# Kernel optimization log

Measured on AMD Instinct MI355X. Metric: run time of the kernel, lower is better.

The kernel has to match this reference:

```python
import jax, jax.numpy as jnp
import numpy as np

N_NODES = 50000
N_EDGES = 800000
IN_DIM = 128
HID = 96
OUT_DIM = 128
N_LAYERS = 3


def setup_inputs() -> dict:
    key = jax.random.key(0)
    ks = jax.random.split(key, 10)
    x = jax.random.normal(ks[0], (N_NODES, IN_DIM), dtype=jnp.float32)
    edge_index = jax.random.randint(ks[1], (2, N_EDGES), 0, N_NODES, dtype=jnp.int32)
    s = 1.0 / np.sqrt(IN_DIM)
    W_in = jax.random.uniform(ks[2], (HID, IN_DIM), jnp.float32, -s, s)
    b_in = jax.random.uniform(ks[3], (HID,), jnp.float32, -s, s)
    sh = 1.0 / np.sqrt(HID)
    W_layers = jax.random.uniform(ks[4], (N_LAYERS, HID, HID), jnp.float32, -sh, sh)
    b_layers = jax.random.uniform(ks[5], (N_LAYERS, HID), jnp.float32, -sh, sh)
    sc = 1.0 / np.sqrt((N_LAYERS + 1) * HID)
    W_out = jax.random.uniform(ks[6], (OUT_DIM, (N_LAYERS + 1) * HID), jnp.float32, -sc, sc)
    b_out = jax.random.uniform(ks[7], (OUT_DIM,), jnp.float32, -sc, sc)
    return {"x": x, "edge_index": edge_index, "W_in": W_in, "b_in": b_in,
            "W_layers": W_layers, "b_layers": b_layers, "W_out": W_out, "b_out": b_out}


def reference(x, edge_index, W_in, b_in, W_layers, b_layers, W_out, b_out):
    src, dst = edge_index[0], edge_index[1]
    # input projection
    h = x @ W_in.T + b_in  # [N, HID]
    hidden_states = [h]
    for l in range(N_LAYERS):
        # GINConv (eps=0): nn((1+eps)*x_i + sum_{j in N(i)} x_j)
        agg = jax.ops.segment_sum(h[src], dst, num_segments=N_NODES)  # [N, HID]
        h = (h + agg) @ W_layers[l].T + b_layers[l]
        hidden_states.append(h)
    cat = jnp.concatenate(hidden_states, axis=1)  # [N, (L+1)*HID]
    return cat @ W_out.T + b_out
```

## Files before the change

kernel.cpp:

```cpp
#include <hip/hip_runtime.h>

#define NN   50000
#define NE   800000
#define IND  128
#define HIDD 96
#define OUTD 128
#define CATD (4 * HIDD)
#define CAP  64

typedef __attribute__((ext_vector_type(8))) short short8v;
typedef __attribute__((ext_vector_type(4))) float f32x4;

__device__ __forceinline__ ushort f2bf(float f) {
    unsigned u = __float_as_uint(f);
    u = (u + 0x7FFFu + ((u >> 16) & 1u)) >> 16;
    return (ushort)u;
}
__device__ __forceinline__ float bf2f(ushort h) {
    return __uint_as_float(((unsigned)h) << 16);
}
__device__ __forceinline__ float blo(unsigned u) { return __uint_as_float(u << 16); }
__device__ __forceinline__ float bhi(unsigned u) { return __uint_as_float(u & 0xffff0000u); }

#define NW_IN  (HIDD * IND)
#define NW_L   (3 * HIDD * HIDD)
#define NW_OUT (OUTD * CATD)
#define NW_ROW (NW_IN + NW_L + NW_OUT)
#define NW_ALL (NW_ROW + NW_L + NW_OUT)

__global__ __launch_bounds__(256)
void wsplit_k(const float* __restrict__ Wi, const float* __restrict__ Wl,
              const float* __restrict__ Wo,
              ushort* __restrict__ whi, ushort* __restrict__ wlo)
{
    int i = blockIdx.x * 256 + threadIdx.x;
    if (i >= NW_ALL) return;
    float v;
    if (i < NW_ROW) {
        if (i < NW_IN)              v = Wi[i];
        else if (i < NW_IN + NW_L)  v = Wl[i - NW_IN];
        else                        v = Wo[i - NW_IN - NW_L];
    } else if (i < NW_ROW + NW_L) {
        int fi = i - NW_ROW;
        int l  = fi / 9216;
        int r  = fi - l * 9216;
        int c  = r / 1536;
        int ks = (r % 1536) / 512;
        int ln = (r % 512) / 8;
        int t  = r & 7;
        int j  = c * 16 + (ln & 15);
        int k  = ks * 32 + 8 * (ln >> 4) + t;
        v = Wl[(l * HIDD + j) * HIDD + k];
    } else {
        int fi = i - NW_ROW - NW_L;
        int c  = fi / 6144;
        int r  = fi - c * 6144;
        int ks = r / 512;
        int ln = (r % 512) / 8;
        int t  = r & 7;
        int j  = c * 16 + (ln & 15);
        int k  = ks * 32 + 8 * (ln >> 4) + t;
        v = Wo[j * CATD + k];
    }
    ushort h = f2bf(v);
    whi[i] = h;
    wlo[i] = f2bf(v - bf2f(h));
}

template<int K, int NCOLS, int ROWS, bool ACCUM>
__global__ __launch_bounds__(256)
void mgemm_k(const float* __restrict__ A,
             const ushort* __restrict__ Whi, const ushort* __restrict__ Wlo,
             int wstride, const float* __restrict__ bias,
             float* __restrict__ C, int cstride, int nrows)
{
    constexpr int ST  = K + 8;
    constexpr int KS  = K / 32;
    constexpr int TRP = (ROWS / 16) / 2;
    constexpr int TCP = (NCOLS / 16) / 2;
    constexpr int CPR = K / 8;

    __shared__ __align__(16) ushort sWh[NCOLS * ST];
    __shared__ __align__(16) ushort sWl[NCOLS * ST];

    const int tid  = threadIdx.x;
    const int w    = tid >> 6;
    const int l    = tid & 63;
    const int lr   = l & 15;
    const int lg   = l >> 4;
    const int row0 = blockIdx.x * ROWS;

    for (int idx = tid; idx < NCOLS * CPR; idx += 256) {
        int j = idx / CPR, c = idx - j * CPR;
        *(uint4*)&sWh[j * ST + c * 8] = *(const uint4*)&Whi[(long)j * wstride + c * 8];
        *(uint4*)&sWl[j * ST + c * 8] = *(const uint4*)&Wlo[(long)j * wstride + c * 8];
    }

    short8v Ah[TRP][KS], Al[TRP][KS];
#pragma unroll
    for (int i = 0; i < TRP; i++) {
        const int row = row0 + ((w >> 1) + 2 * i) * 16 + lr;
#pragma unroll
        for (int ks = 0; ks < KS; ks++) {
            float4 r0 = make_float4(0.f, 0.f, 0.f, 0.f);
            float4 r1 = make_float4(0.f, 0.f, 0.f, 0.f);
            if (row < nrows) {
                const float* p = &A[(long)row * K + ks * 32 + 8 * lg];
                r0 = *(const float4*)p;
                r1 = *(const float4*)(p + 4);
            }
            const float f[8] = {r0.x, r0.y, r0.z, r0.w, r1.x, r1.y, r1.z, r1.w};
            short8v hi, lo;
#pragma unroll
            for (int t = 0; t < 8; t++) {
                ushort h = f2bf(f[t]);
                hi[t] = (short)h;
                lo[t] = (short)f2bf(f[t] - bf2f(h));
            }
            Ah[i][ks] = hi;
            Al[i][ks] = lo;
        }
    }
    __syncthreads();

#pragma unroll
    for (int j = 0; j < TCP; j++) {
        const int colb = ((w & 1) + 2 * j) * 16;
        short8v Bh[KS], Bl[KS];
#pragma unroll
        for (int ks = 0; ks < KS; ks++) {
            Bh[ks] = *(const short8v*)&sWh[(colb + lr) * ST + ks * 32 + 8 * lg];
            Bl[ks] = *(const short8v*)&sWl[(colb + lr) * ST + ks * 32 + 8 * lg];
        }
        const float bv = bias ? bias[colb + lr] : 0.f;
#pragma unroll
        for (int i = 0; i < TRP; i++) {
            f32x4 acc = {bv, bv, bv, bv};
#pragma unroll
            for (int ks = 0; ks < KS; ks++) {
                acc = __builtin_amdgcn_mfma_f32_16x16x32_bf16(Ah[i][ks], Bh[ks], acc, 0, 0, 0);
                acc = __builtin_amdgcn_mfma_f32_16x16x32_bf16(Ah[i][ks], Bl[ks], acc, 0, 0, 0);
                acc = __builtin_amdgcn_mfma_f32_16x16x32_bf16(Al[i][ks], Bh[ks], acc, 0, 0, 0);
            }
#pragma unroll
            for (int p = 0; p < 4; p++) {
                const int row = row0 + ((w >> 1) + 2 * i) * 16 + 4 * lg + p;
                if (row < nrows) {
                    float* cp = &C[(long)row * cstride + colb + lr];
                    if (ACCUM) *cp += acc[p];
                    else       *cp  = acc[p];
                }
            }
        }
    }
}

__global__ __launch_bounds__(256)
void fillb_k(const int* __restrict__ ei, int* __restrict__ cursor,
             ushort* __restrict__ bucket)
{
    unsigned int e = blockIdx.x * 256u + threadIdx.x;
    if (e < (unsigned int)NE) {
        int s = ei[e];
        int d = ei[NE + e];
        int pos = atomicAdd(&cursor[d], 1);
        if (pos < CAP) bucket[(long)d * CAP + pos] = (ushort)s;
    }
}

__global__ __launch_bounds__(256)
void hcvt_k(const float* __restrict__ hf, int istride, ushort* __restrict__ hb)
{
    int idx = blockIdx.x * 256 + threadIdx.x;
    if (idx >= NN * (HIDD / 8)) return;
    int row = idx / (HIDD / 8);
    int c   = (idx - row * (HIDD / 8)) * 8;
    const float* p = &hf[(long)row * istride + c];
    const float4 r0 = *(const float4*)p;
    const float4 r1 = *(const float4*)(p + 4);
    uint4 o;
    o.x = (unsigned)f2bf(r0.x) | ((unsigned)f2bf(r0.y) << 16);
    o.y = (unsigned)f2bf(r0.z) | ((unsigned)f2bf(r0.w) << 16);
    o.z = (unsigned)f2bf(r1.x) | ((unsigned)f2bf(r1.y) << 16);
    o.w = (unsigned)f2bf(r1.z) | ((unsigned)f2bf(r1.w) << 16);
    *(uint4*)&hb[(long)row * HIDD + c] = o;
}

#define FROWS 32
#define FAST  100

__global__ __launch_bounds__(256)
void flayer_k(const float* __restrict__ hf_in, int istride,
              const ushort* __restrict__ hb_in,
              const int* __restrict__ cursor, const ushort* __restrict__ bucket,
              const ushort* __restrict__ fWhi, const ushort* __restrict__ fWlo,
              const float* __restrict__ bias,
              float* __restrict__ hf_out, int ostride,
              ushort* __restrict__ hb_out)
{
    __shared__ __align__(16) float sA[FROWS * FAST];

    const int tid = threadIdx.x;
    const int n0  = blockIdx.x * FROWS;

    {
        const int i  = tid >> 3;
        const int st = tid & 7;
        const int n  = n0 + i;
        float4 s0 = make_float4(0.f, 0.f, 0.f, 0.f);
        float4 s1 = s0, s2 = s0;
        if (n < NN) {
            const float* hp = &hf_in[(long)n * istride + st * 12];
            s0 = ((const float4*)hp)[0];
            s1 = *(const float4*)(hp + 4);
            s2 = *(const float4*)(hp + 8);
            int cnt = cursor[n];
            if (cnt > CAP) cnt = CAP;
            const ushort* bp = &bucket[(long)n * CAP];
            const ushort* hbb = hb_in + st * 12;
#define ACCB(q)                                                              \
            { const uint2 a = *(const uint2*)(q);                            \
              const uint2 b = *(const uint2*)((q) + 4);                      \
              const uint2 c = *(const uint2*)((q) + 8);                      \
              s0.x += blo(a.x); s0.y += bhi(a.x); s0.z += blo(a.y); s0.w += bhi(a.y); \
              s1.x += blo(b.x); s1.y += bhi(b.x); s1.z += blo(b.y); s1.w += bhi(b.y); \
              s2.x += blo(c.x); s2.y += bhi(c.x); s2.z += blo(c.y); s2.w += bhi(c.y); }
            int e = 0;
            for (; e + 1 < cnt; e += 2) {
                const unsigned id2 = *(const unsigned*)&bp[e];
                const ushort* q0 = &hbb[(long)(id2 & 0xffffu) * HIDD];
                const ushort* q1 = &hbb[(long)(id2 >> 16) * HIDD];
                ACCB(q0); ACCB(q1);
            }
            if (e < cnt) {
                const ushort* q = &hbb[(long)bp[e] * HIDD];
                ACCB(q);
            }
#undef ACCB
        }
        float* ap = &sA[i * FAST + st * 12];
        ((float4*)ap)[0] = s0;
        ((float4*)ap)[1] = s1;
        ((float4*)ap)[2] = s2;
    }
    __syncthreads();

    const int w  = tid >> 6;
    const int l  = tid & 63;
    const int lr = l & 15;
    const int lg = l >> 4;
    const int tr = w >> 1;

    short8v Ah[3], Al[3];
#pragma unroll
    for (int ks = 0; ks < 3; ks++) {
        const float* ap = &sA[(tr * 16 + lr) * FAST + ks * 32 + 8 * lg];
        const float4 r0 = ((const float4*)ap)[0];
        const float4 r1 = ((const float4*)ap)[1];
        const float f[8] = {r0.x, r0.y, r0.z, r0.w, r1.x, r1.y, r1.z, r1.w};
        short8v hi, lo;
#pragma unroll
        for (int t = 0; t < 8; t++) {
            ushort h = f2bf(f[t]);
            hi[t] = (short)h;
            lo[t] = (short)f2bf(f[t] - bf2f(h));
        }
        Ah[ks] = hi;
        Al[ks] = lo;
    }

#pragma unroll
    for (int j = 0; j < 3; j++) {
        const int c    = (w & 1) + 2 * j;
        const int colb = c * 16;
        short8v Bh[3], Bl[3];
#pragma unroll
        for (int ks = 0; ks < 3; ks++) {
            Bh[ks] = *(const short8v*)&fWhi[((c * 3 + ks) * 64 + l) * 8];
            Bl[ks] = *(const short8v*)&fWlo[((c * 3 + ks) * 64 + l) * 8];
        }
        const float bv = bias[colb + lr];
        f32x4 acc = {bv, bv, bv, bv};
#pragma unroll
        for (int ks = 0; ks < 3; ks++) {
            acc = __builtin_amdgcn_mfma_f32_16x16x32_bf16(Ah[ks], Bh[ks], acc, 0, 0, 0);
            acc = __builtin_amdgcn_mfma_f32_16x16x32_bf16(Ah[ks], Bl[ks], acc, 0, 0, 0);
            acc = __builtin_amdgcn_mfma_f32_16x16x32_bf16(Al[ks], Bh[ks], acc, 0, 0, 0);
        }
#pragma unroll
        for (int p = 0; p < 4; p++) {
            const int row = n0 + tr * 16 + 4 * lg + p;
            if (row < NN) {
                hf_out[(long)row * ostride + colb + lr] = acc[p];
                if (hb_out)
                    hb_out[(long)row * HIDD + colb + lr] = f2bf(acc[p]);
            }
        }
    }
}

__global__ __launch_bounds__(256)
void fgemm_k(const float* __restrict__ cat, const ushort* __restrict__ fOhi,
             const ushort* __restrict__ fOlo, const float* __restrict__ bias,
             float* __restrict__ out)
{
    const int tid  = threadIdx.x;
    const int w    = tid >> 6;
    const int l    = tid & 63;
    const int lr   = l & 15;
    const int lg   = l >> 4;
    const int row0 = blockIdx.x * 32;
    const int rt   = w >> 1;
    const int ch   = w & 1;
    const int arow = row0 + rt * 16 + lr;

    f32x4 acc[4];
#pragma unroll
    for (int j = 0; j < 4; j++) {
        const float bv = bias[(ch + 2 * j) * 16 + lr];
        acc[j] = (f32x4){bv, bv, bv, bv};
    }

#pragma unroll 4
    for (int ks = 0; ks < 12; ks++) {
        float4 r0 = make_float4(0.f, 0.f, 0.f, 0.f);
        float4 r1 = make_float4(0.f, 0.f, 0.f, 0.f);
        if (arow < NN) {
            const float* p = &cat[(long)arow * CATD + ks * 32 + 8 * lg];
            r0 = *(const float4*)p;
            r1 = *(const float4*)(p + 4);
        }
        const float f[8] = {r0.x, r0.y, r0.z, r0.w, r1.x, r1.y, r1.z, r1.w};
        short8v Ah, Al;
#pragma unroll
        for (int t = 0; t < 8; t++) {
            ushort h = f2bf(f[t]);
            Ah[t] = (short)h;
            Al[t] = (short)f2bf(f[t] - bf2f(h));
        }
#pragma unroll
        for (int j = 0; j < 4; j++) {
            const int c = ch + 2 * j;
            const short8v Bh = *(const short8v*)&fOhi[((c * 12 + ks) * 64 + l) * 8];
            const short8v Bl = *(const short8v*)&fOlo[((c * 12 + ks) * 64 + l) * 8];
            acc[j] = __builtin_amdgcn_mfma_f32_16x16x32_bf16(Ah, Bh, acc[j], 0, 0, 0);
            acc[j] = __builtin_amdgcn_mfma_f32_16x16x32_bf16(Ah, Bl, acc[j], 0, 0, 0);
            acc[j] = __builtin_amdgcn_mfma_f32_16x16x32_bf16(Al, Bh, acc[j], 0, 0, 0);
        }
    }

#pragma unroll
    for (int p = 0; p < 4; p++) {
        const int row = row0 + rt * 16 + 4 * lg + p;
        if (row < NN) {
#pragma unroll
            for (int j = 0; j < 4; j++)
                out[(long)row * OUTD + (ch + 2 * j) * 16 + lr] = acc[j][p];
        }
    }
}

extern "C" void kernel_launch(void* const* d_in, const int* in_sizes, int n_in,
                              void* d_out, int out_size, void* d_ws, size_t ws_size,
                              hipStream_t stream)
{
    const float* x  = (const float*)d_in[0];
    const int*   ei = (const int*)  d_in[1];
    const float* Wi = (const float*)d_in[2];
    const float* bi = (const float*)d_in[3];
    const float* Wl = (const float*)d_in[4];
    const float* bl = (const float*)d_in[5];
    const float* Wo = (const float*)d_in[6];
    const float* bo = (const float*)d_in[7];
    float* out = (float*)d_out;

    char* p = (char*)d_ws;
    int* cursor    = (int*)p;              p += ((size_t)NN * 4 + 255) & ~255ull;
    ushort* bucket = (ushort*)p;           p += ((size_t)NN * CAP * 2 + 255) & ~255ull;
    ushort* whi = (ushort*)p;              p += ((size_t)NW_ALL * 2 + 255) & ~255ull;
    ushort* wlo = (ushort*)p;              p += ((size_t)NW_ALL * 2 + 255) & ~255ull;
    ushort* hbfA = (ushort*)p;             p += ((size_t)NN * HIDD * 2 + 255) & ~255ull;
    ushort* hbfB = (ushort*)p;             p += ((size_t)NN * HIDD * 2 + 255) & ~255ull;
    float* big  = (float*)p;
    const size_t used = (size_t)(p - (char*)d_ws);
    const bool catpath = (ws_size >= used + (size_t)NN * CATD * 4);

    const ushort* whi_in = whi;
    const ushort* wlo_in = wlo;
    const ushort* whi_o  = whi + NW_IN + NW_L;
    const ushort* wlo_o  = wlo + NW_IN + NW_L;
    const ushort* fLhi   = whi + NW_ROW;
    const ushort* fLlo   = wlo + NW_ROW;
    const ushort* fOhi   = whi + NW_ROW + NW_L;
    const ushort* fOlo   = wlo + NW_ROW + NW_L;

    hipLaunchKernelGGL(wsplit_k, dim3((NW_ALL + 255) / 256), dim3(256), 0, stream,
                       Wi, Wl, Wo, whi, wlo);
    hipMemsetAsync(cursor, 0, (size_t)NN * sizeof(int), stream);
    hipLaunchKernelGGL(fillb_k, dim3((NE + 255) / 256), dim3(256), 0, stream,
                       ei, cursor, bucket);

    if (catpath) {
        float* cat = big;
        hipLaunchKernelGGL((mgemm_k<IND, HIDD, 32, false>),
                           dim3((NN + 31) / 32), dim3(256), 0, stream,
                           x, whi_in, wlo_in, IND, bi, cat, CATD, NN);
        hipLaunchKernelGGL(hcvt_k, dim3((NN * (HIDD / 8) + 255) / 256), dim3(256), 0, stream,
                           cat, CATD, hbfA);
        hipLaunchKernelGGL(flayer_k, dim3((NN + FROWS - 1) / FROWS), dim3(256), 0, stream,
                           cat, CATD, hbfA, cursor, bucket,
                           fLhi, fLlo, bl, cat + HIDD, CATD, hbfB);
        hipLaunchKernelGGL(flayer_k, dim3((NN + FROWS - 1) / FROWS), dim3(256), 0, stream,
                           cat + HIDD, CATD, hbfB, cursor, bucket,
                           fLhi + 9216, fLlo + 9216, bl + HIDD,
                           cat + 2 * HIDD, CATD, hbfA);
        hipLaunchKernelGGL(flayer_k, dim3((NN + FROWS - 1) / FROWS), dim3(256), 0, stream,
                           cat + 2 * HIDD, CATD, hbfA, cursor, bucket,
                           fLhi + 2 * 9216, fLlo + 2 * 9216, bl + 2 * HIDD,
                           cat + 3 * HIDD, CATD, (ushort*)nullptr);
        hipLaunchKernelGGL(fgemm_k, dim3((NN + 31) / 32), dim3(256), 0, stream,
                           cat, fOhi, fOlo, bo, out);
    } else {
        float* hA = big;
        float* hB = hA + (size_t)NN * HIDD;
        hipLaunchKernelGGL((mgemm_k<IND, HIDD, 32, false>),
                           dim3((NN + 31) / 32), dim3(256), 0, stream,
                           x, whi_in, wlo_in, IND, bi, hA, HIDD, NN);
        hipLaunchKernelGGL((mgemm_k<HIDD, OUTD, 64, false>),
                           dim3((NN + 63) / 64), dim3(256), 0, stream,
                           hA, whi_o, wlo_o, CATD, bo, out, OUTD, NN);
        hipLaunchKernelGGL(hcvt_k, dim3((NN * (HIDD / 8) + 255) / 256), dim3(256), 0, stream,
                           hA, HIDD, hbfA);
        const float* hsrc = hA;  float* hdst = hB;
        ushort* bsrc = hbfA;     ushort* bdst = hbfB;
        for (int l = 0; l < 3; l++) {
            hipLaunchKernelGGL(flayer_k, dim3((NN + FROWS - 1) / FROWS), dim3(256), 0, stream,
                               hsrc, HIDD, bsrc, cursor, bucket,
                               fLhi + (size_t)l * 9216, fLlo + (size_t)l * 9216,
                               bl + (size_t)l * HIDD, hdst, HIDD,
                               (l < 2) ? bdst : (ushort*)nullptr);
            hipLaunchKernelGGL((mgemm_k<HIDD, OUTD, 64, true>),
                               dim3((NN + 63) / 64), dim3(256), 0, stream,
                               hdst, whi_o + (size_t)(l + 1) * HIDD,
                               wlo_o + (size_t)(l + 1) * HIDD, CATD,
                               (const float*)nullptr, out, OUTD, NN);
            const float* t = hsrc; hsrc = hdst; hdst = (float*)t;
            ushort* tb = bsrc; bsrc = bdst; bdst = tb;
        }
    }
}
```

Before: 316.9 us.

## Bin edges by destination before bucket fill and fuse bf16 conversion into GEMM

Replaces the direct per-edge atomic bucket fill with a multi-pass scheme: a shared-memory histogram over 49 destination bins, a scan, a block-local binning pass that writes packed (dst,src) edges grouped by bin, then a per-bin fill so cursor atomics and bucket writes stay localized. It also removes the separate hcvt kernel by having the input-projection GEMM write the bf16 copy directly. The cost is four extra launches, an extra 3.2 MB intermediate array, and a bucket fill limited to 49 blocks. Packing src into 16 bits only works because node ids are below 65536.

Result: slower. 334.9 us (+5.7%).

```diff
diff --git a/kernel.cpp b/kernel.cpp
--- a/kernel.cpp
+++ b/kernel.cpp
@@ -7,6 +7,8 @@
 #define OUTD 128
 #define CATD (4 * HIDD)
 #define CAP  64
+#define NBIN 49
+#define BCH  4096
 
 typedef __attribute__((ext_vector_type(8))) short short8v;
 typedef __attribute__((ext_vector_type(4))) float f32x4;
@@ -72,7 +74,8 @@
 void mgemm_k(const float* __restrict__ A,
              const ushort* __restrict__ Whi, const ushort* __restrict__ Wlo,
              int wstride, const float* __restrict__ bias,
-             float* __restrict__ C, int cstride, int nrows)
+             float* __restrict__ C, int cstride, int nrows,
+             ushort* __restrict__ bfC)
 {
     constexpr int ST  = K + 8;
     constexpr int KS  = K / 32;
@@ -149,6 +152,8 @@
                     float* cp = &C[(long)row * cstride + colb + lr];
                     if (ACCUM) *cp += acc[p];
                     else       *cp  = acc[p];
+                    if (bfC)
+                        bfC[(long)row * HIDD + colb + lr] = f2bf(acc[p]);
                 }
             }
         }
@@ -156,34 +161,106 @@
 }
 
 __global__ __launch_bounds__(256)
-void fillb_k(const int* __restrict__ ei, int* __restrict__ cursor,
-             ushort* __restrict__ bucket)
-{
-    unsigned int e = blockIdx.x * 256u + threadIdx.x;
-    if (e < (unsigned int)NE) {
-        int s = ei[e];
-        int d = ei[NE + e];
-        int pos = atomicAdd(&cursor[d], 1);
+void hist_k(const int* __restrict__ ei, int* __restrict__ binCount)
+{
+    __shared__ int h[NBIN];
+    for (int b = threadIdx.x; b < NBIN; b += 256) h[b] = 0;
+    __syncthreads();
+    int e0 = (blockIdx.x * 256 + threadIdx.x) * 4;
+    if (e0 + 4 <= NE) {
+        const int4 d4 = *(const int4*)&ei[NE + e0];
+        atomicAdd(&h[d4.x >> 10], 1);
+        atomicAdd(&h[d4.y >> 10], 1);
+        atomicAdd(&h[d4.z >> 10], 1);
+        atomicAdd(&h[d4.w >> 10], 1);
+    }
+    __syncthreads();
+    for (int b = threadIdx.x; b < NBIN; b += 256)
+        if (h[b]) atomicAdd(&binCount[b], h[b]);
+}
+
+__global__ __launch_bounds__(64)
+void binscan_k(const int* __restrict__ binCount, int* __restrict__ binStart,
+               int* __restrict__ binCursor)
+{
+    __shared__ int v[64];
+    const int t = threadIdx.x;
+    int x = (t < NBIN) ? binCount[t] : 0;
+    v[t] = x;
+    __syncthreads();
+    for (int off = 1; off < 64; off <<= 1) {
+        int tmp = (t >= off) ? v[t - off] : 0;
+        __syncthreads();
+        v[t] += tmp;
+        __syncthreads();
+    }
+    if (t < NBIN) { int ex = v[t] - x; binStart[t] = ex; binCursor[t] = ex; }
+    if (t == NBIN - 1) binStart[NBIN] = v[t];
+}
+
+__global__ __launch_bounds__(256)
+void binfill_k(const int* __restrict__ ei, int* __restrict__ binCursor,
+               unsigned* __restrict__ binned)
+{
+    __shared__ unsigned sbuf[BCH];
+    __shared__ int lcnt[NBIN], lstart[NBIN], lcur[NBIN], gbase[NBIN];
+    const int tid  = threadIdx.x;
+    const int base = blockIdx.x * BCH;
+
+    for (int b = tid; b < NBIN; b += 256) { lcnt[b] = 0; lcur[b] = 0; }
+    __syncthreads();
+
+    unsigned ent[16];
+#pragma unroll
+    for (int r = 0; r < 16; r++) {
+        const int e = base + r * 256 + tid;
+        if (e < NE) {
+            const int s = ei[e];
+            const int d = ei[NE + e];
+            ent[r] = ((unsigned)d << 16) | (unsigned)s;
+            atomicAdd(&lcnt[d >> 10], 1);
+        } else {
+            ent[r] = 0xffffffffu;
+        }
+    }
+    __syncthreads();
+    if (tid == 0) {
+        int run = 0;
+        for (int b = 0; b < NBIN; b++) { lstart[b] = run; run += lcnt[b]; }
+    }
+    __syncthreads();
+    if (tid < NBIN) gbase[tid] = atomicAdd(&binCursor[tid], lcnt[tid]);
+    __syncthreads();
+#pragma unroll
+    for (int r = 0; r < 16; r++) {
+        if (ent[r] != 0xffffffffu) {
+            const int bin = ent[r] >> 26;
+            const int pos = atomicAdd(&lcur[bin], 1);
+            sbuf[lstart[bin] + pos] = ent[r];
+        }
+    }
+    __syncthreads();
+    const int total = lstart[NBIN - 1] + lcnt[NBIN - 1];
+    for (int i = tid; i < total; i += 256) {
+        const unsigned e = sbuf[i];
+        const int bin = e >> 26;
+        binned[gbase[bin] + (i - lstart[bin])] = e;
+    }
+}
+
+__global__ __launch_bounds__(1024)
+void bfill_k(const unsigned* __restrict__ binned, const int* __restrict__ binStart,
+             int* __restrict__ cursor, ushort* __restrict__ bucket)
+{
+    const int b   = blockIdx.x;
+    const int beg = binStart[b], end = binStart[b + 1];
+    for (int i = beg + threadIdx.x; i < end; i += 1024) {
+        const unsigned e = binned[i];
+        const int d = e >> 16;
+        const int s = e & 0xffffu;
+        const int pos = atomicAdd(&cursor[d], 1);
         if (pos < CAP) bucket[(long)d * CAP + pos] = (ushort)s;
     }
-}
-
-__global__ __launch_bounds__(256)
-void hcvt_k(const float* __restrict__ hf, int istride, ushort* __restrict__ hb)
-{
-    int idx = blockIdx.x * 256 + threadIdx.x;
-    if (idx >= NN * (HIDD / 8)) return;
-    int row = idx / (HIDD / 8);
-    int c   = (idx - row * (HIDD / 8)) * 8;
-    const float* p = &hf[(long)row * istride + c];
-    const float4 r0 = *(const float4*)p;
-    const float4 r1 = *(const float4*)(p + 4);
-    uint4 o;
-    o.x = (unsigned)f2bf(r0.x) | ((unsigned)f2bf(r0.y) << 16);
-    o.y = (unsigned)f2bf(r0.z) | ((unsigned)f2bf(r0.w) << 16);
-    o.z = (unsigned)f2bf(r1.x) | ((unsigned)f2bf(r1.y) << 16);
-    o.w = (unsigned)f2bf(r1.z) | ((unsigned)f2bf(r1.w) << 16);
-    *(uint4*)&hb[(long)row * HIDD + c] = o;
 }
 
 #define FROWS 32
@@ -375,8 +452,12 @@
     float* out = (float*)d_out;
 
     char* p = (char*)d_ws;
-    int* cursor    = (int*)p;              p += ((size_t)NN * 4 + 255) & ~255ull;
+    int* cursor    = (int*)p;              p += ((size_t)(NN + 2 * NBIN + NBIN + 1) * 4 + 255) & ~255ull;
+    int* binCount  = cursor + NN;
+    int* binCursor = binCount + NBIN;
+    int* binStart  = binCursor + NBIN;
     ushort* bucket = (ushort*)p;           p += ((size_t)NN * CAP * 2 + 255) & ~255ull;
+    unsigned* binned = (unsigned*)p;       p += ((size_t)NE * 4 + 255) & ~255ull;
     ushort* whi = (ushort*)p;              p += ((size_t)NW_ALL * 2 + 255) & ~255ull;
     ushort* wlo = (ushort*)p;              p += ((size_t)NW_ALL * 2 + 255) & ~255ull;
     ushort* hbfA = (ushort*)p;             p += ((size_t)NN * HIDD * 2 + 255) & ~255ull;
@@ -396,17 +477,21 @@
 
     hipLaunchKernelGGL(wsplit_k, dim3((NW_ALL + 255) / 256), dim3(256), 0, stream,
                        Wi, Wl, Wo, whi, wlo);
-    hipMemsetAsync(cursor, 0, (size_t)NN * sizeof(int), stream);
-    hipLaunchKernelGGL(fillb_k, dim3((NE + 255) / 256), dim3(256), 0, stream,
-                       ei, cursor, bucket);
+    hipMemsetAsync(cursor, 0, (size_t)(NN + 2 * NBIN) * sizeof(int), stream);
+    hipLaunchKernelGGL(hist_k, dim3((NE / 4 + 255) / 256), dim3(256), 0, stream,
+                       ei, binCount);
+    hipLaunchKernelGGL(binscan_k, dim3(1), dim3(64), 0, stream,
+                       binCount, binStart, binCursor);
+    hipLaunchKernelGGL(binfill_k, dim3((NE + BCH - 1) / BCH), dim3(256), 0, stream,
+                       ei, binCursor, binned);
+    hipLaunchKernelGGL(bfill_k, dim3(NBIN), dim3(1024), 0, stream,
+                       binned, binStart, cursor, bucket);
 
     if (catpath) {
         float* cat = big;
         hipLaunchKernelGGL((mgemm_k<IND, HIDD, 32, false>),
                            dim3((NN + 31) / 32), dim3(256), 0, stream,
-                           x, whi_in, wlo_in, IND, bi, cat, CATD, NN);
-        hipLaunchKernelGGL(hcvt_k, dim3((NN * (HIDD / 8) + 255) / 256), dim3(256), 0, stream,
-                           cat, CATD, hbfA);
+                           x, whi_in, wlo_in, IND, bi, cat, CATD, NN, hbfA);
         hipLaunchKernelGGL(flayer_k, dim3((NN + FROWS - 1) / FROWS), dim3(256), 0, stream,
                            cat, CATD, hbfA, cursor, bucket,
                            fLhi, fLlo, bl, cat + HIDD, CATD, hbfB);
@@ -425,12 +510,10 @@
         float* hB = hA + (size_t)NN * HIDD;
         hipLaunchKernelGGL((mgemm_k<IND, HIDD, 32, false>),
                            dim3((NN + 31) / 32), dim3(256), 0, stream,
-                           x, whi_in, wlo_in, IND, bi, hA, HIDD, NN);
+                           x, whi_in, wlo_in, IND, bi, hA, HIDD, NN, hbfA);
         hipLaunchKernelGGL((mgemm_k<HIDD, OUTD, 64, false>),
                            dim3((NN + 63) / 64), dim3(256), 0, stream,
-                           hA, whi_o, wlo_o, CATD, bo, out, OUTD, NN);
-        hipLaunchKernelGGL(hcvt_k, dim3((NN * (HIDD / 8) + 255) / 256), dim3(256), 0, stream,
-                           hA, HIDD, hbfA);
+                           hA, whi_o, wlo_o, CATD, bo, out, OUTD, NN, (ushort*)nullptr);
         const float* hsrc = hA;  float* hdst = hB;
         ushort* bsrc = hbfA;     ushort* bdst = hbfB;
         for (int l = 0; l < 3; l++) {
@@ -443,7 +526,7 @@
                                dim3((NN + 63) / 64), dim3(256), 0, stream,
                                hdst, whi_o + (size_t)(l + 1) * HIDD,
                                wlo_o + (size_t)(l + 1) * HIDD, CATD,
-                               (const float*)nullptr, out, OUTD, NN);
+                               (const float*)nullptr, out, OUTD, NN, (ushort*)nullptr);
             const float* t = hsrc; hsrc = hdst; hdst = (float*)t;
             ushort* tb = bsrc; bsrc = bdst; bdst = tb;
         }
```

## Store concatenated hidden states as bf16 hi/lo pairs and drop conversion kernel

Applied to the files above, without the earlier changes.

Replaces the fp32 concatenated hidden-state buffer with two bf16 buffers (hi and lo split) written directly by the GEMM and layer kernels. This removes the separate hcvt conversion pass and the per-element fp32-to-bf16 splitting in the output GEMM. The output GEMM is retiled to 64 rows per block with 4x2 MFMA accumulators per wave to reuse B fragments. Neighbor gathers now read from the strided hi buffer inside the cat layout, which may reduce locality compared to the old packed 96-wide bf16 copy.

Result: slower. 341.9 us (+7.9%).

```diff
diff --git a/kernel.cpp b/kernel.cpp
--- a/kernel.cpp
+++ b/kernel.cpp
@@ -72,7 +72,8 @@
 void mgemm_k(const float* __restrict__ A,
              const ushort* __restrict__ Whi, const ushort* __restrict__ Wlo,
              int wstride, const float* __restrict__ bias,
-             float* __restrict__ C, int cstride, int nrows)
+             float* __restrict__ C, int cstride, int nrows,
+             ushort* __restrict__ bfHi, ushort* __restrict__ bfLo, int bstride)
 {
     constexpr int ST  = K + 8;
     constexpr int KS  = K / 32;
@@ -146,9 +147,17 @@
             for (int p = 0; p < 4; p++) {
                 const int row = row0 + ((w >> 1) + 2 * i) * 16 + 4 * lg + p;
                 if (row < nrows) {
-                    float* cp = &C[(long)row * cstride + colb + lr];
-                    if (ACCUM) *cp += acc[p];
-                    else       *cp  = acc[p];
+                    if (C) {
+                        float* cp = &C[(long)row * cstride + colb + lr];
+                        if (ACCUM) *cp += acc[p];
+                        else       *cp  = acc[p];
+                    }
+                    if (bfHi) {
+                        ushort h = f2bf(acc[p]);
+                        bfHi[(long)row * bstride + colb + lr] = h;
+                        if (bfLo)
+                            bfLo[(long)row * bstride + colb + lr] = f2bf(acc[p] - bf2f(h));
+                    }
                 }
             }
         }
@@ -168,35 +177,19 @@
     }
 }
 
-__global__ __launch_bounds__(256)
-void hcvt_k(const float* __restrict__ hf, int istride, ushort* __restrict__ hb)
-{
-    int idx = blockIdx.x * 256 + threadIdx.x;
-    if (idx >= NN * (HIDD / 8)) return;
-    int row = idx / (HIDD / 8);
-    int c   = (idx - row * (HIDD / 8)) * 8;
-    const float* p = &hf[(long)row * istride + c];
-    const float4 r0 = *(const float4*)p;
-    const float4 r1 = *(const float4*)(p + 4);
-    uint4 o;
-    o.x = (unsigned)f2bf(r0.x) | ((unsigned)f2bf(r0.y) << 16);
-    o.y = (unsigned)f2bf(r0.z) | ((unsigned)f2bf(r0.w) << 16);
-    o.z = (unsigned)f2bf(r1.x) | ((unsigned)f2bf(r1.y) << 16);
-    o.w = (unsigned)f2bf(r1.z) | ((unsigned)f2bf(r1.w) << 16);
-    *(uint4*)&hb[(long)row * HIDD + c] = o;
-}
-
 #define FROWS 32
 #define FAST  100
 
 __global__ __launch_bounds__(256)
-void flayer_k(const float* __restrict__ hf_in, int istride,
-              const ushort* __restrict__ hb_in,
+void flayer_k(const float* __restrict__ hf_in, int ifstride,
+              const ushort* __restrict__ hiIn, const ushort* __restrict__ loIn,
+              int ibstride,
               const int* __restrict__ cursor, const ushort* __restrict__ bucket,
               const ushort* __restrict__ fWhi, const ushort* __restrict__ fWlo,
               const float* __restrict__ bias,
-              float* __restrict__ hf_out, int ostride,
-              ushort* __restrict__ hb_out)
+              float* __restrict__ hf_out, int ofstride,
+              ushort* __restrict__ hiOut, ushort* __restrict__ loOut,
+              int obstride)
 {
     __shared__ __align__(16) float sA[FROWS * FAST];
 
@@ -210,14 +203,31 @@
         float4 s0 = make_float4(0.f, 0.f, 0.f, 0.f);
         float4 s1 = s0, s2 = s0;
         if (n < NN) {
-            const float* hp = &hf_in[(long)n * istride + st * 12];
-            s0 = ((const float4*)hp)[0];
-            s1 = *(const float4*)(hp + 4);
-            s2 = *(const float4*)(hp + 8);
+            if (hf_in) {
+                const float* hp = &hf_in[(long)n * ifstride + st * 12];
+                s0 = ((const float4*)hp)[0];
+                s1 = *(const float4*)(hp + 4);
+                s2 = *(const float4*)(hp + 8);
+            } else {
+                const ushort* hq = &hiIn[(long)n * ibstride + st * 12];
+                const ushort* lq = &loIn[(long)n * ibstride + st * 12];
+                const uint2 a = *(const uint2*)hq;
+                const uint2 b = *(const uint2*)(hq + 4);
+                const uint2 c = *(const uint2*)(hq + 8);
+                const uint2 d = *(const uint2*)lq;
+                const uint2 e = *(const uint2*)(lq + 4);
+                const uint2 f = *(const uint2*)(lq + 8);
+                s0 = make_float4(blo(a.x) + blo(d.x), bhi(a.x) + bhi(d.x),
+                                 blo(a.y) + blo(d.y), bhi(a.y) + bhi(d.y));
+                s1 = make_float4(blo(b.x) + blo(e.x), bhi(b.x) + bhi(e.x),
+                                 blo(b.y) + blo(e.y), bhi(b.y) + bhi(e.y));
+                s2 = make_float4(blo(c.x) + blo(f.x), bhi(c.x) + bhi(f.x),
+                                 blo(c.y) + blo(f.y), bhi(c.y) + bhi(f.y));
+            }
             int cnt = cursor[n];
             if (cnt > CAP) cnt = CAP;
             const ushort* bp = &bucket[(long)n * CAP];
-            const ushort* hbb = hb_in + st * 12;
+            const ushort* hbb = hiIn + st * 12;
 #define ACCB(q)                                                              \
             { const uint2 a = *(const uint2*)(q);                            \
               const uint2 b = *(const uint2*)((q) + 4);                      \
@@ -228,12 +238,12 @@
             int e = 0;
             for (; e + 1 < cnt; e += 2) {
                 const unsigned id2 = *(const unsigned*)&bp[e];
-                const ushort* q0 = &hbb[(long)(id2 & 0xffffu) * HIDD];
-                const ushort* q1 = &hbb[(long)(id2 >> 16) * HIDD];
+                const ushort* q0 = &hbb[(long)(id2 & 0xffffu) * ibstride];
+                const ushort* q1 = &hbb[(long)(id2 >> 16) * ibstride];
                 ACCB(q0); ACCB(q1);
             }
             if (e < cnt) {
-                const ushort* q = &hbb[(long)bp[e] * HIDD];
+                const ushort* q = &hbb[(long)bp[e] * ibstride];
                 ACCB(q);
             }
 #undef ACCB
@@ -291,71 +301,78 @@
         for (int p = 0; p < 4; p++) {
             const int row = n0 + tr * 16 + 4 * lg + p;
             if (row < NN) {
-                hf_out[(long)row * ostride + colb + lr] = acc[p];
-                if (hb_out)
-                    hb_out[(long)row * HIDD + colb + lr] = f2bf(acc[p]);
+                if (hf_out)
+                    hf_out[(long)row * ofstride + colb + lr] = acc[p];
+                if (hiOut) {
+                    ushort h = f2bf(acc[p]);
+                    hiOut[(long)row * obstride + colb + lr] = h;
+                    if (loOut)
+                        loOut[(long)row * obstride + colb + lr] = f2bf(acc[p] - bf2f(h));
+                }
             }
         }
     }
 }
 
 __global__ __launch_bounds__(256)
-void fgemm_k(const float* __restrict__ cat, const ushort* __restrict__ fOhi,
-             const ushort* __restrict__ fOlo, const float* __restrict__ bias,
-             float* __restrict__ out)
+void fgemm_k(const ushort* __restrict__ catHi, const ushort* __restrict__ catLo,
+             const ushort* __restrict__ fOhi, const ushort* __restrict__ fOlo,
+             const float* __restrict__ bias, float* __restrict__ out)
 {
     const int tid  = threadIdx.x;
     const int w    = tid >> 6;
     const int l    = tid & 63;
     const int lr   = l & 15;
     const int lg   = l >> 4;
-    const int row0 = blockIdx.x * 32;
-    const int rt   = w >> 1;
-    const int ch   = w & 1;
-    const int arow = row0 + rt * 16 + lr;
-
-    f32x4 acc[4];
-#pragma unroll
-    for (int j = 0; j < 4; j++) {
-        const float bv = bias[(ch + 2 * j) * 16 + lr];
-        acc[j] = (f32x4){bv, bv, bv, bv};
-    }
-
-#pragma unroll 4
+    const int row0 = blockIdx.x * 64;
+
+    f32x4 acc[4][2];
+#pragma unroll
+    for (int cj = 0; cj < 2; cj++) {
+        const float bv = bias[(2 * w + cj) * 16 + lr];
+#pragma unroll
+        for (int rt = 0; rt < 4; rt++) acc[rt][cj] = (f32x4){bv, bv, bv, bv};
+    }
+
+#pragma unroll 3
     for (int ks = 0; ks < 12; ks++) {
-        float4 r0 = make_float4(0.f, 0.f, 0.f, 0.f);
-        float4 r1 = make_float4(0.f, 0.f, 0.f, 0.f);
-        if (arow < NN) {
-            const float* p = &cat[(long)arow * CATD + ks * 32 + 8 * lg];
-            r0 = *(const float4*)p;
-            r1 = *(const float4*)(p + 4);
-        }
-        const float f[8] = {r0.x, r0.y, r0.z, r0.w, r1.x, r1.y, r1.z, r1.w};
-        short8v Ah, Al;
-#pragma unroll
-        for (int t = 0; t < 8; t++) {
-            ushort h = f2bf(f[t]);
-            Ah[t] = (short)h;
-            Al[t] = (short)f2bf(f[t] - bf2f(h));
-        }
-#pragma unroll
-        for (int j = 0; j < 4; j++) {
-            const int c = ch + 2 * j;
+        short8v Ah[4], Al[4];
+#pragma unroll
+        for (int rt = 0; rt < 4; rt++) {
+            const int row = row0 + rt * 16 + lr;
+            if (row < NN) {
+                const long off = (long)row * CATD + ks * 32 + 8 * lg;
+                Ah[rt] = *(const short8v*)&catHi[off];
+                Al[rt] = *(const short8v*)&catLo[off];
+            } else {
+                Ah[rt] = (short8v){0,0,0,0,0,0,0,0};
+                Al[rt] = (short8v){0,0,0,0,0,0,0,0};
+            }
+        }
+#pragma unroll
+        for (int cj = 0; cj < 2; cj++) {
+            const int c = 2 * w + cj;
             const short8v Bh = *(const short8v*)&fOhi[((c * 12 + ks) * 64 + l) * 8];
             const short8v Bl = *(const short8v*)&fOlo[((c * 12 + ks) * 64 + l) * 8];
-            acc[j] = __builtin_amdgcn_mfma_f32_16x16x32_bf16(Ah, Bh, acc[j], 0, 0, 0);
-            acc[j] = __builtin_amdgcn_mfma_f32_16x16x32_bf16(Ah, Bl, acc[j], 0, 0, 0);
-            acc[j] = __builtin_amdgcn_mfma_f32_16x16x32_bf16(Al, Bh, acc[j], 0, 0, 0);
-        }
-    }
-
-#pragma unroll
-    for (int p = 0; p < 4; p++) {
-        const int row = row0 + rt * 16 + 4 * lg + p;
-        if (row < NN) {
-#pragma unroll
-            for (int j = 0; j < 4; j++)
-                out[(long)row * OUTD + (ch + 2 * j) * 16 + lr] = acc[j][p];
+#pragma unroll
+            for (int rt = 0; rt < 4; rt++) {
+                acc[rt][cj] = __builtin_amdgcn_mfma_f32_16x16x32_bf16(Ah[rt], Bh, acc[rt][cj], 0, 0, 0);
+                acc[rt][cj] = __builtin_amdgcn_mfma_f32_16x16x32_bf16(Ah[rt], Bl, acc[rt][cj], 0, 0, 0);
+                acc[rt][cj] = __builtin_amdgcn_mfma_f32_16x16x32_bf16(Al[rt], Bh, acc[rt][cj], 0, 0, 0);
+            }
+        }
+    }
+
+#pragma unroll
+    for (int rt = 0; rt < 4; rt++) {
+#pragma unroll
+        for (int p = 0; p < 4; p++) {
+            const int row = row0 + rt * 16 + 4 * lg + p;
+            if (row < NN) {
+#pragma unroll
+                for (int cj = 0; cj < 2; cj++)
+                    out[(long)row * OUTD + (2 * w + cj) * 16 + lr] = acc[rt][cj][p];
+            }
         }
     }
 }
@@ -379,11 +396,9 @@
     ushort* bucket = (ushort*)p;           p += ((size_t)NN * CAP * 2 + 255) & ~255ull;
     ushort* whi = (ushort*)p;              p += ((size_t)NW_ALL * 2 + 255) & ~255ull;
     ushort* wlo = (ushort*)p;              p += ((size_t)NW_ALL * 2 + 255) & ~255ull;
-    ushort* hbfA = (ushort*)p;             p += ((size_t)NN * HIDD * 2 + 255) & ~255ull;
-    ushort* hbfB = (ushort*)p;             p += ((size_t)NN * HIDD * 2 + 255) & ~255ull;
-    float* big  = (float*)p;
+    char* big = p;
     const size_t used = (size_t)(p - (char*)d_ws);
-    const bool catpath = (ws_size >= used + (size_t)NN * CATD * 4);
+    const bool catpath = (ws_size >= used + 2 * (size_t)NN * CATD * 2);
 
     const ushort* whi_in = whi;
     const ushort* wlo_in = wlo;
@@ -401,49 +416,54 @@
                        ei, cursor, bucket);
 
     if (catpath) {
-        float* cat = big;
+        ushort* catHi = (ushort*)big;
+        ushort* catLo = catHi + (size_t)NN * CATD;
         hipLaunchKernelGGL((mgemm_k<IND, HIDD, 32, false>),
                            dim3((NN + 31) / 32), dim3(256), 0, stream,
-                           x, whi_in, wlo_in, IND, bi, cat, CATD, NN);
-        hipLaunchKernelGGL(hcvt_k, dim3((NN * (HIDD / 8) + 255) / 256), dim3(256), 0, stream,
-                           cat, CATD, hbfA);
-        hipLaunchKernelGGL(flayer_k, dim3((NN + FROWS - 1) / FROWS), dim3(256), 0, stream,
-                           cat, CATD, hbfA, cursor, bucket,
-                           fLhi, fLlo, bl, cat + HIDD, CATD, hbfB);
-        hipLaunchKernelGGL(flayer_k, dim3((NN + FROWS - 1) / FROWS), dim3(256), 0, stream,
-                           cat + HIDD, CATD, hbfB, cursor, bucket,
-                           fLhi + 9216, fLlo + 9216, bl + HIDD,
-                           cat + 2 * HIDD, CATD, hbfA);
-        hipLaunchKernelGGL(flayer_k, dim3((NN + FROWS - 1) / FROWS), dim3(256), 0, stream,
-                           cat + 2 * HIDD, CATD, hbfA, cursor, bucket,
-                           fLhi + 2 * 9216, fLlo + 2 * 9216, bl + 2 * HIDD,
-                           cat + 3 * HIDD, CATD, (ushort*)nullptr);
-        hipLaunchKernelGGL(fgemm_k, dim3((NN + 31) / 32), dim3(256), 0, stream,
-                           cat, fOhi, fOlo, bo, out);
+                           x, whi_in, wlo_in, IND, bi,
+                           (float*)nullptr, 0, NN, catHi, catLo, CATD);
+        for (int l = 0; l < 3; l++) {
+            hipLaunchKernelGGL(flayer_k, dim3((NN + FROWS - 1) / FROWS), dim3(256), 0, stream,
+                               (const float*)nullptr, 0,
+                               catHi + (size_t)l * HIDD, catLo + (size_t)l * HIDD, CATD,
+                               cursor, bucket,
+                               fLhi + (size_t)l * 9216, fLlo + (size_t)l * 9216,
+                               bl + (size_t)l * HIDD,
+                               (float*)nullptr, 0,
+                               catHi + (size_t)(l + 1) * HIDD,
+                               catLo + (size_t)(l + 1) * HIDD, CATD);
+        }
+        hipLaunchKernelGGL(fgemm_k, dim3((NN + 63) / 64), dim3(256), 0, stream,
+                           catHi, catLo, fOhi, fOlo, bo, out);
     } else {
-        float* hA = big;
+        float* hA = (float*)big;
         float* hB = hA + (size_t)NN * HIDD;
+        ushort* hbfA = (ushort*)(hB + (size_t)NN * HIDD);
+        ushort* hbfB = hbfA + (size_t)NN * HIDD;
         hipLaunchKernelGGL((mgemm_k<IND, HIDD, 32, false>),
                            dim3((NN + 31) / 32), dim3(256), 0, stream,
-                           x, whi_in, wlo_in, IND, bi, hA, HIDD, NN);
+                           x, whi_in, wlo_in, IND, bi, hA, HIDD, NN,
+                           hbfA, (ushort*)nullptr, HIDD);
         hipLaunchKernelGGL((mgemm_k<HIDD, OUTD, 64, false>),
                            dim3((NN + 63) / 64), dim3(256), 0, stream,
-                           hA, whi_o, wlo_o, CATD, bo, out, OUTD, NN);
-        hipLaunchKernelGGL(hcvt_k, dim3((NN * (HIDD / 8) + 255) / 256), dim3(256), 0, stream,
-                           hA, HIDD, hbfA);
+                           hA, whi_o, wlo_o, CATD, bo, out, OUTD, NN,
+                           (ushort*)nullptr, (ushort*)nullptr, 0);
         const float* hsrc = hA;  float* hdst = hB;
         ushort* bsrc = hbfA;     ushort* bdst = hbfB;
         for (int l = 0; l < 3; l++) {
             hipLaunchKernelGGL(flayer_k, dim3((NN + FROWS - 1) / FROWS), dim3(256), 0, stream,
-                               hsrc, HIDD, bsrc, cursor, bucket,
+                               hsrc, HIDD, bsrc, (const ushort*)nullptr, HIDD,
+                               cursor, bucket,
                                fLhi + (size_t)l * 9216, fLlo + (size_t)l * 9216,
-                               bl + (size_t)l * HIDD, hdst, HIDD,
-                               (l < 2) ? bdst : (ushort*)nullptr);
+                               bl + (size_t)l * HIDD,
+                               hdst, HIDD,
+                               (l < 2) ? bdst : (ushort*)nullptr, (ushort*)nullptr, HIDD);
             hipLaunchKernelGGL((mgemm_k<HIDD, OUTD, 64, true>),
                                dim3((NN + 63) / 64), dim3(256), 0, stream,
                                hdst, whi_o + (size_t)(l + 1) * HIDD,
                                wlo_o + (size_t)(l + 1) * HIDD, CATD,
-                               (const float*)nullptr, out, OUTD, NN);
+                               (const float*)nullptr, out, OUTD, NN,
+                               (ushort*)nullptr, (ushort*)nullptr, 0);
             const float* t = hsrc; hsrc = hdst; hdst = (float*)t;
             ushort* tb = bsrc; bsrc = bdst; bdst = tb;
         }
```

## Store concatenated hidden states as bf16 and drop the separate conversion kernel

Applied to the files above, without the earlier changes.

The input-projection GEMM and each GIN layer now write a bf16 copy of their output straight into a bf16 concat buffer, so the hcvt conversion kernel and the fp32 concat buffer are removed. The final output GEMM reads bf16 activations directly and skips the low-part split of the activations, going from three to two MFMAs per step. The fp32 hidden copy is kept only for the self term of the next layer. This cuts memory traffic and MFMA work but drops the activation low-order correction in the output projection, which lowers accuracy.

Result: faster. 300.0 us (-5.3%).

```diff
diff --git a/kernel.cpp b/kernel.cpp
--- a/kernel.cpp
+++ b/kernel.cpp
@@ -72,7 +72,8 @@
 void mgemm_k(const float* __restrict__ A,
              const ushort* __restrict__ Whi, const ushort* __restrict__ Wlo,
              int wstride, const float* __restrict__ bias,
-             float* __restrict__ C, int cstride, int nrows)
+             float* __restrict__ C, int cstride, int nrows,
+             ushort* __restrict__ bfHi, int bstride)
 {
     constexpr int ST  = K + 8;
     constexpr int KS  = K / 32;
@@ -146,9 +147,13 @@
             for (int p = 0; p < 4; p++) {
                 const int row = row0 + ((w >> 1) + 2 * i) * 16 + 4 * lg + p;
                 if (row < nrows) {
-                    float* cp = &C[(long)row * cstride + colb + lr];
-                    if (ACCUM) *cp += acc[p];
-                    else       *cp  = acc[p];
+                    if (C) {
+                        float* cp = &C[(long)row * cstride + colb + lr];
+                        if (ACCUM) *cp += acc[p];
+                        else       *cp  = acc[p];
+                    }
+                    if (bfHi)
+                        bfHi[(long)row * bstride + colb + lr] = f2bf(acc[p]);
                 }
             }
         }
@@ -168,35 +173,17 @@
     }
 }
 
-__global__ __launch_bounds__(256)
-void hcvt_k(const float* __restrict__ hf, int istride, ushort* __restrict__ hb)
-{
-    int idx = blockIdx.x * 256 + threadIdx.x;
-    if (idx >= NN * (HIDD / 8)) return;
-    int row = idx / (HIDD / 8);
-    int c   = (idx - row * (HIDD / 8)) * 8;
-    const float* p = &hf[(long)row * istride + c];
-    const float4 r0 = *(const float4*)p;
-    const float4 r1 = *(const float4*)(p + 4);
-    uint4 o;
-    o.x = (unsigned)f2bf(r0.x) | ((unsigned)f2bf(r0.y) << 16);
-    o.y = (unsigned)f2bf(r0.z) | ((unsigned)f2bf(r0.w) << 16);
-    o.z = (unsigned)f2bf(r1.x) | ((unsigned)f2bf(r1.y) << 16);
-    o.w = (unsigned)f2bf(r1.z) | ((unsigned)f2bf(r1.w) << 16);
-    *(uint4*)&hb[(long)row * HIDD + c] = o;
-}
-
 #define FROWS 32
 #define FAST  100
 
 __global__ __launch_bounds__(256)
-void flayer_k(const float* __restrict__ hf_in, int istride,
-              const ushort* __restrict__ hb_in,
+void flayer_k(const float* __restrict__ hf_in,
+              const ushort* __restrict__ hiIn, int ibstride,
               const int* __restrict__ cursor, const ushort* __restrict__ bucket,
               const ushort* __restrict__ fWhi, const ushort* __restrict__ fWlo,
               const float* __restrict__ bias,
-              float* __restrict__ hf_out, int ostride,
-              ushort* __restrict__ hb_out)
+              float* __restrict__ hf_out,
+              ushort* __restrict__ hiOut, int obstride)
 {
     __shared__ __align__(16) float sA[FROWS * FAST];
 
@@ -210,14 +197,14 @@
         float4 s0 = make_float4(0.f, 0.f, 0.f, 0.f);
         float4 s1 = s0, s2 = s0;
         if (n < NN) {
-            const float* hp = &hf_in[(long)n * istride + st * 12];
+            const float* hp = &hf_in[(long)n * HIDD + st * 12];
             s0 = ((const float4*)hp)[0];
             s1 = *(const float4*)(hp + 4);
             s2 = *(const float4*)(hp + 8);
             int cnt = cursor[n];
             if (cnt > CAP) cnt = CAP;
             const ushort* bp = &bucket[(long)n * CAP];
-            const ushort* hbb = hb_in + st * 12;
+            const ushort* hbb = hiIn + st * 12;
 #define ACCB(q)                                                              \
             { const uint2 a = *(const uint2*)(q);                            \
               const uint2 b = *(const uint2*)((q) + 4);                      \
@@ -228,12 +215,12 @@
             int e = 0;
             for (; e + 1 < cnt; e += 2) {
                 const unsigned id2 = *(const unsigned*)&bp[e];
-                const ushort* q0 = &hbb[(long)(id2 & 0xffffu) * HIDD];
-                const ushort* q1 = &hbb[(long)(id2 >> 16) * HIDD];
+                const ushort* q0 = &hbb[(long)(id2 & 0xffffu) * ibstride];
+                const ushort* q1 = &hbb[(long)(id2 >> 16) * ibstride];
                 ACCB(q0); ACCB(q1);
             }
             if (e < cnt) {
-                const ushort* q = &hbb[(long)bp[e] * HIDD];
+                const ushort* q = &hbb[(long)bp[e] * ibstride];
                 ACCB(q);
             }
 #undef ACCB
@@ -291,18 +278,18 @@
         for (int p = 0; p < 4; p++) {
             const int row = n0 + tr * 16 + 4 * lg + p;
             if (row < NN) {
-                hf_out[(long)row * ostride + colb + lr] = acc[p];
-                if (hb_out)
-                    hb_out[(long)row * HIDD + colb + lr] = f2bf(acc[p]);
-            }
-        }
-    }
-}
-
-__global__ __launch_bounds__(256)
-void fgemm_k(const float* __restrict__ cat, const ushort* __restrict__ fOhi,
-             const ushort* __restrict__ fOlo, const float* __restrict__ bias,
-             float* __restrict__ out)
+                if (hf_out)
+                    hf_out[(long)row * HIDD + colb + lr] = acc[p];
+                hiOut[(long)row * obstride + colb + lr] = f2bf(acc[p]);
+            }
+        }
+    }
+}
+
+__global__ __launch_bounds__(256)
+void fgemm_k(const ushort* __restrict__ catBf,
+             const ushort* __restrict__ fOhi, const ushort* __restrict__ fOlo,
+             const float* __restrict__ bias, float* __restrict__ out)
 {
     const int tid  = threadIdx.x;
     const int w    = tid >> 6;
@@ -323,21 +310,9 @@
 
 #pragma unroll 4
     for (int ks = 0; ks < 12; ks++) {
-        float4 r0 = make_float4(0.f, 0.f, 0.f, 0.f);
-        float4 r1 = make_float4(0.f, 0.f, 0.f, 0.f);
-        if (arow < NN) {
-            const float* p = &cat[(long)arow * CATD + ks * 32 + 8 * lg];
-            r0 = *(const float4*)p;
-            r1 = *(const float4*)(p + 4);
-        }
-        const float f[8] = {r0.x, r0.y, r0.z, r0.w, r1.x, r1.y, r1.z, r1.w};
-        short8v Ah, Al;
-#pragma unroll
-        for (int t = 0; t < 8; t++) {
-            ushort h = f2bf(f[t]);
-            Ah[t] = (short)h;
-            Al[t] = (short)f2bf(f[t] - bf2f(h));
-        }
+        short8v Ah = (short8v){0,0,0,0,0,0,0,0};
+        if (arow < NN)
+            Ah = *(const short8v*)&catBf[(long)arow * CATD + ks * 32 + 8 * lg];
 #pragma unroll
         for (int j = 0; j < 4; j++) {
             const int c = ch + 2 * j;
@@ -345,7 +320,6 @@
             const short8v Bl = *(const short8v*)&fOlo[((c * 12 + ks) * 64 + l) * 8];
             acc[j] = __builtin_amdgcn_mfma_f32_16x16x32_bf16(Ah, Bh, acc[j], 0, 0, 0);
             acc[j] = __builtin_amdgcn_mfma_f32_16x16x32_bf16(Ah, Bl, acc[j], 0, 0, 0);
-            acc[j] = __builtin_amdgcn_mfma_f32_16x16x32_bf16(Al, Bh, acc[j], 0, 0, 0);
         }
     }
 
@@ -379,16 +353,12 @@
     ushort* bucket = (ushort*)p;           p += ((size_t)NN * CAP * 2 + 255) & ~255ull;
     ushort* whi = (ushort*)p;              p += ((size_t)NW_ALL * 2 + 255) & ~255ull;
     ushort* wlo = (ushort*)p;              p += ((size_t)NW_ALL * 2 + 255) & ~255ull;
-    ushort* hbfA = (ushort*)p;             p += ((size_t)NN * HIDD * 2 + 255) & ~255ull;
-    ushort* hbfB = (ushort*)p;             p += ((size_t)NN * HIDD * 2 + 255) & ~255ull;
-    float* big  = (float*)p;
-    const size_t used = (size_t)(p - (char*)d_ws);
-    const bool catpath = (ws_size >= used + (size_t)NN * CATD * 4);
+    ushort* catBf = (ushort*)p;            p += ((size_t)NN * CATD * 2 + 255) & ~255ull;
+    float* hA = (float*)p;                 p += ((size_t)NN * HIDD * 4 + 255) & ~255ull;
+    float* hB = (float*)p;                 p += ((size_t)NN * HIDD * 4 + 255) & ~255ull;
 
     const ushort* whi_in = whi;
     const ushort* wlo_in = wlo;
-    const ushort* whi_o  = whi + NW_IN + NW_L;
-    const ushort* wlo_o  = wlo + NW_IN + NW_L;
     const ushort* fLhi   = whi + NW_ROW;
     const ushort* fLlo   = wlo + NW_ROW;
     const ushort* fOhi   = whi + NW_ROW + NW_L;
@@ -400,52 +370,22 @@
     hipLaunchKernelGGL(fillb_k, dim3((NE + 255) / 256), dim3(256), 0, stream,
                        ei, cursor, bucket);
 
-    if (catpath) {
-        float* cat = big;
-        hipLaunchKernelGGL((mgemm_k<IND, HIDD, 32, false>),
-                           dim3((NN + 31) / 32), dim3(256), 0, stream,
-                           x, whi_in, wlo_in, IND, bi, cat, CATD, NN);
-        hipLaunchKernelGGL(hcvt_k, dim3((NN * (HIDD / 8) + 255) / 256), dim3(256), 0, stream,
-                           cat, CATD, hbfA);
+    hipLaunchKernelGGL((mgemm_k<IND, HIDD, 32, false>),
+                       dim3((NN + 31) / 32), dim3(256), 0, stream,
+                       x, whi_in, wlo_in, IND, bi, hA, HIDD, NN, catBf, CATD);
+
+    const float* hsrc = hA;  float* hdst = hB;
+    for (int l = 0; l < 3; l++) {
         hipLaunchKernelGGL(flayer_k, dim3((NN + FROWS - 1) / FROWS), dim3(256), 0, stream,
-                           cat, CATD, hbfA, cursor, bucket,
-                           fLhi, fLlo, bl, cat + HIDD, CATD, hbfB);
-        hipLaunchKernelGGL(flayer_k, dim3((NN + FROWS - 1) / FROWS), dim3(256), 0, stream,
-                           cat + HIDD, CATD, hbfB, cursor, bucket,
-                           fLhi + 9216, fLlo + 9216, bl + HIDD,
-                           cat + 2 * HIDD, CATD, hbfA);
-        hipLaunchKernelGGL(flayer_k, dim3((NN + FROWS - 1) / FROWS), dim3(256), 0, stream,
-                           cat + 2 * HIDD, CATD, hbfA, cursor, bucket,
-                           fLhi + 2 * 9216, fLlo + 2 * 9216, bl + 2 * HIDD,
-                           cat + 3 * HIDD, CATD, (ushort*)nullptr);
-        hipLaunchKernelGGL(fgemm_k, dim3((NN + 31) / 32), dim3(256), 0, stream,
-                           cat, fOhi, fOlo, bo, out);
-    } else {
-        float* hA = big;
-        float* hB = hA + (size_t)NN * HIDD;
-        hipLaunchKernelGGL((mgemm_k<IND, HIDD, 32, false>),
-                           dim3((NN + 31) / 32), dim3(256), 0, stream,
-                           x, whi_in, wlo_in, IND, bi, hA, HIDD, NN);
-        hipLaunchKernelGGL((mgemm_k<HIDD, OUTD, 64, false>),
-                           dim3((NN + 63) / 64), dim3(256), 0, stream,
-                           hA, whi_o, wlo_o, CATD, bo, out, OUTD, NN);
-        hipLaunchKernelGGL(hcvt_k, dim3((NN * (HIDD / 8) + 255) / 256), dim3(256), 0, stream,
-                           hA, HIDD, hbfA);
-        const float* hsrc = hA;  float* hdst = hB;
-        ushort* bsrc = hbfA;     ushort* bdst = hbfB;
-        for (int l = 0; l < 3; l++) {
-            hipLaunchKernelGGL(flayer_k, dim3((NN + FROWS - 1) / FROWS), dim3(256), 0, stream,
-                               hsrc, HIDD, bsrc, cursor, bucket,
-                               fLhi + (size_t)l * 9216, fLlo + (size_t)l * 9216,
-                               bl + (size_t)l * HIDD, hdst, HIDD,
-                               (l < 2) ? bdst : (ushort*)nullptr);
-            hipLaunchKernelGGL((mgemm_k<HIDD, OUTD, 64, true>),
-                               dim3((NN + 63) / 64), dim3(256), 0, stream,
-                               hdst, whi_o + (size_t)(l + 1) * HIDD,
-                               wlo_o + (size_t)(l + 1) * HIDD, CATD,
-                               (const float*)nullptr, out, OUTD, NN);
-            const float* t = hsrc; hsrc = hdst; hdst = (float*)t;
-            ushort* tb = bsrc; bsrc = bdst; bdst = tb;
-        }
-    }
-}
+                           hsrc, catBf + (size_t)l * HIDD, CATD,
+                           cursor, bucket,
+                           fLhi + (size_t)l * 9216, fLlo + (size_t)l * 9216,
+                           bl + (size_t)l * HIDD,
+                           (l < 2) ? hdst : (float*)nullptr,
+                           catBf + (size_t)(l + 1) * HIDD, CATD);
+        const float* t = hsrc; hsrc = hdst; hdst = (float*)t;
+    }
+
+    hipLaunchKernelGGL(fgemm_k, dim3((NN + 31) / 32), dim3(256), 0, stream,
+                       catBf, fOhi, fOlo, bo, out);
+}
```
